# Kernel tuning notes

Hardware: AMD Instinct MI355X
Metric: run time of the kernel (lower is better)

## Reference

```python
import jax, jax.numpy as jnp
import numpy as np

EPS = 1e-5


def gcn_conv(x, src, dst, n_nodes, W, b):
    # x: [B, N, Fin]; src/dst: [E+N] (self loops included); W: [Fout, Fin]
    h = jnp.einsum('bnf,of->bno', x, W)                      # [B, N, Fout]
    deg = jnp.zeros((n_nodes,), h.dtype).at[dst].add(1.0)    # in-degree of A+I
    dinv = jnp.where(deg > 0, 1.0 / jnp.sqrt(deg), 0.0)
    norm = dinv[src] * dinv[dst]                             # [E+N]
    msg = h[:, src, :] * norm[None, :, None]                 # gather along node axis
    out = jnp.zeros_like(h).at[:, dst, :].add(msg)           # scatter-add aggregate
    return out + b


def batchnorm_nodes(x, gamma, beta):
    # torch BatchNorm1d(N) on [B, N, C]: channel axis is N, stats over (B, C)
    mean = jnp.mean(x, axis=(0, 2), keepdims=True)
    var = jnp.mean(jnp.square(x - mean), axis=(0, 2), keepdims=True)
    xn = (x - mean) * jax.lax.rsqrt(var + EPS)
    return xn * gamma[None, :, None] + beta[None, :, None]


def setup_inputs() -> dict:
    key = jax.random.key(0)
    ks = jax.random.split(key, 20)
    B, N, FIN, D, OUT, E = 4096, 64, 67, 2048, 2, 512
    s = 0.1
    d = {}
    d['x_fingerprints'] = jax.random.normal(ks[0], (B, D), jnp.float32)
    d['x_node_features'] = jax.random.normal(ks[1], (B, N, FIN), jnp.float32)
    d['edge_list'] = jax.random.randint(ks[2], (2, E), 0, N)
    d['W1'] = jax.random.normal(ks[3], (64, FIN), jnp.float32) * s
    d['b1'] = jax.random.normal(ks[4], (64,), jnp.float32) * s
    d['g1'] = 1.0 + jax.random.normal(ks[5], (N,), jnp.float32) * s
    d['be1'] = jax.random.normal(ks[6], (N,), jnp.float32) * s
    d['W2'] = jax.random.normal(ks[7], (32, 64), jnp.float32) * s
    d['b2'] = jax.random.normal(ks[8], (32,), jnp.float32) * s
    d['g2'] = 1.0 + jax.random.normal(ks[9], (N,), jnp.float32) * s
    d['be2'] = jax.random.normal(ks[10], (N,), jnp.float32) * s
    d['Wl1'] = jax.random.normal(ks[11], (400, D), jnp.float32) * (s / 4)
    d['bl1'] = jax.random.normal(ks[12], (400,), jnp.float32) * s
    d['Wl2'] = jax.random.normal(ks[13], (64, 400), jnp.float32) * s
    d['bl2'] = jax.random.normal(ks[14], (64,), jnp.float32) * s
    d['Wfc'] = jax.random.normal(ks[15], (OUT, 96), jnp.float32) * s
    d['bfc'] = jax.random.normal(ks[16], (OUT,), jnp.float32) * s
    return d


def reference(x_fingerprints, x_node_features, edge_list, W1, b1, g1, be1,
              W2, b2, g2, be2, Wl1, bl1, Wl2, bl2, Wfc, bfc):
    B, N, _ = x_node_features.shape
    loops = jnp.arange(N)
    src = jnp.concatenate([edge_list[0], loops])  # add self loops (GCNConv default)
    dst = jnp.concatenate([edge_list[1], loops])
    g = gcn_conv(x_node_features, src, dst, N, W1, b1)
    g = jax.nn.relu(batchnorm_nodes(g, g1, be1))
    g = gcn_conv(g, src, dst, N, W2, b2)
    g = jax.nn.relu(batchnorm_nodes(g, g2, be2))           # [B, N, 32]
    pooled = jnp.max(g, axis=1)                             # global_max_pool -> [B, 32]
    h = jax.nn.relu(x_fingerprints @ Wl1.T + bl1)
    h = jax.nn.relu(h @ Wl2.T + bl2)                        # [B, 64]
    out = jnp.concatenate([pooled, h], axis=1) @ Wfc.T + bfc
    return out
```

## Files before the change

### kernel.cpp

```cpp
#include <hip/hip_runtime.h>
#include <hip/hip_bf16.h>
#include <math.h>

typedef __bf16 bf16;
typedef __attribute__((ext_vector_type(8))) __bf16 bf16x8;
typedef __attribute__((ext_vector_type(4))) __bf16 bf16x4;
typedef __attribute__((ext_vector_type(4))) float f32x4;

#define EPSBN 1e-5f
#define B_    4096
#define N_    64
#define FIN_  67
#define E_    512
#define NSLOT 128

__device__ inline bf16x8 pack8(f32x4 lo, f32x4 hi) {
    bf16x8 r;
    r[0] = (bf16)lo[0]; r[1] = (bf16)lo[1]; r[2] = (bf16)lo[2]; r[3] = (bf16)lo[3];
    r[4] = (bf16)hi[0]; r[5] = (bf16)hi[1]; r[6] = (bf16)hi[2]; r[7] = (bf16)hi[3];
    return r;
}

__global__ __launch_bounds__(256) void k0_prep(const int* __restrict__ edge,
    const float* __restrict__ W1, const float* __restrict__ W2,
    float* __restrict__ partials,
    bf16* __restrict__ an_hi, bf16* __restrict__ an_lo,
    bf16* __restrict__ wpad,
    bf16* __restrict__ w2pad)
{
    int tid = threadIdx.x;
    for (int i = blockIdx.x * 256 + tid; i < NSLOT * 64 * 4; i += gridDim.x * 256)
        partials[i] = 0.f;
    if (blockIdx.x == 1) {
        for (int i = tid; i < 64 * 104; i += 256) {
            int n = i / 104, f = i % 104;
            wpad[i] = (f < FIN_) ? (bf16)W1[n * FIN_ + f] : (bf16)0.f;
        }
        return;
    }
    if (blockIdx.x == 2) {
        for (int i = tid; i < 32 * 72; i += 256) {
            int o = i / 72, f = i % 72;
            w2pad[i] = (f < 64) ? (bf16)W2[o * 64 + f] : (bf16)0.f;
        }
        return;
    }
    if (blockIdx.x != 0) return;

    __shared__ float An[64 * 64];
    __shared__ int ssrc[E_], sdst[E_];
    __shared__ int deg[N_];
    __shared__ float dinv[N_];
    for (int i = tid; i < 64 * 64; i += 256) An[i] = 0.f;
    for (int i = tid; i < E_; i += 256) { ssrc[i] = edge[i]; sdst[i] = edge[E_ + i]; }
    if (tid < N_) deg[tid] = 1;
    __syncthreads();
    for (int i = tid; i < E_; i += 256) atomicAdd(&deg[sdst[i]], 1);
    __syncthreads();
    if (tid < N_) dinv[tid] = rsqrtf((float)deg[tid]);
    __syncthreads();
    for (int i = tid; i < E_; i += 256) {
        int s = ssrc[i], d = sdst[i];
        atomicAdd(&An[d * 64 + s], dinv[s] * dinv[d]);
    }
    if (tid < N_) atomicAdd(&An[tid * 64 + tid], dinv[tid] * dinv[tid]);
    __syncthreads();
    for (int i = tid; i < 64 * 64; i += 256) {
        float v = An[i];
        bf16 h = (bf16)v;
        an_hi[i] = h;
        an_lo[i] = (bf16)(v - (float)h);
    }
}

__global__ __launch_bounds__(256, 3) void k1_gcn1(
    const float* __restrict__ x,
    const float* __restrict__ b1,
    const bf16* __restrict__ an_hi, const bf16* __restrict__ an_lo,
    const bf16* __restrict__ wpad,
    bf16* __restrict__ g1out,
    float* __restrict__ part1)
{
    __shared__ union {
        float xraw[4352];
        struct { bf16 hhi[64 * 72]; bf16 hlo[64 * 72]; } h;
    } u;
    __shared__ bf16 ost[64 * 72];

    int tid = threadIdx.x;
    int w = tid >> 6, lane = tid & 63, q = lane >> 4, r15 = lane & 15;
    int arow = w * 16 + r15;

    bf16x8 wf[3][4];
#pragma unroll
    for (int kt = 0; kt < 3; ++kt)
#pragma unroll
        for (int nt = 0; nt < 4; ++nt)
            wf[kt][nt] = *(const bf16x8*)&wpad[(nt * 16 + r15) * 104 + kt * 32 + q * 8];

    const bf16* ahp = an_hi + arow * 64 + q * 8;
    const bf16* alp = an_lo + arow * 64 + q * 8;
    bf16x8 Ah0 = *(const bf16x8*)ahp;
    bf16x8 Ah1 = *(const bf16x8*)(ahp + 32);
    bf16x8 Al0 = *(const bf16x8*)alp;
    bf16x8 Al1 = *(const bf16x8*)(alp + 32);

    float bc[4];
#pragma unroll
    for (int nt = 0; nt < 4; ++nt) bc[nt] = b1[nt * 16 + r15];

    size_t b0 = (size_t)blockIdx.x * 4;
    const f32x4* xb4 = (const f32x4*)(x + b0 * 4288);

    f32x4 pre0 = xb4[tid], pre1 = xb4[tid + 256], pre2 = xb4[tid + 512], pre3 = xb4[tid + 768];
    f32x4 pre4 = {0.f, 0.f, 0.f, 0.f};
    if (tid < 48) pre4 = xb4[tid + 1024];

    f32x4* xl4 = (f32x4*)u.xraw;
    f32x4 z4 = {0.f, 0.f, 0.f, 0.f};

#pragma unroll 1
    for (int g = 0; g < 4; ++g) {
        int b = (int)b0 + g;
        xl4[tid] = pre0; xl4[tid + 256] = pre1; xl4[tid + 512] = pre2; xl4[tid + 768] = pre3;
        if (tid < 48) xl4[tid + 1024] = pre4;
        __syncthreads();

        f32x4 acc[4] = {z4, z4, z4, z4};
        const float* xr = u.xraw + arow * FIN_;
#pragma unroll
        for (int kt = 0; kt < 3; ++kt) {
            bf16x8 a;
            if (kt < 2) {
                int k0 = kt * 32 + q * 8;
#pragma unroll
                for (int j = 0; j < 8; ++j) a[j] = (bf16)xr[k0 + j];
            } else {
#pragma unroll
                for (int j = 0; j < 8; ++j) a[j] = (bf16)0.f;
                if (q == 0) { a[0] = (bf16)xr[64]; a[1] = (bf16)xr[65]; a[2] = (bf16)xr[66]; }
            }
#pragma unroll
            for (int nt = 0; nt < 4; ++nt)
                acc[nt] = __builtin_amdgcn_mfma_f32_16x16x32_bf16(a, wf[kt][nt], acc[nt], 0, 0, 0);
        }
        if (g < 3) {
            const f32x4* xn = xb4 + (size_t)(g + 1) * 1072;
            pre0 = xn[tid]; pre1 = xn[tid + 256]; pre2 = xn[tid + 512]; pre3 = xn[tid + 768];
            if (tid < 48) pre4 = xn[tid + 1024];
        }
        __syncthreads();

        int sbase = w * 16 + q * 4;
#pragma unroll
        for (int nt = 0; nt < 4; ++nt) {
            int c = nt * 16 + r15;
            bf16x4 hi, lo;
#pragma unroll
            for (int r = 0; r < 4; ++r) {
                float v = acc[nt][r];
                bf16 h = (bf16)v;
                hi[r] = h; lo[r] = (bf16)(v - (float)h);
            }
            *(bf16x4*)&u.h.hhi[c * 72 + sbase] = hi;
            *(bf16x4*)&u.h.hlo[c * 72 + sbase] = lo;
        }
        __syncthreads();

        f32x4 acc2[4] = {z4, z4, z4, z4};
#pragma unroll
        for (int kt = 0; kt < 2; ++kt) {
            bf16x8 Ahk = kt ? Ah1 : Ah0;
            bf16x8 Alk = kt ? Al1 : Al0;
#pragma unroll
            for (int nt = 0; nt < 4; ++nt) {
                int o = (nt * 16 + r15) * 72 + kt * 32 + q * 8;
                bf16x8 Hh = *(const bf16x8*)&u.h.hhi[o];
                bf16x8 Hl = *(const bf16x8*)&u.h.hlo[o];
                acc2[nt] = __builtin_amdgcn_mfma_f32_16x16x32_bf16(Ahk, Hh, acc2[nt], 0, 0, 0);
                acc2[nt] = __builtin_amdgcn_mfma_f32_16x16x32_bf16(Ahk, Hl, acc2[nt], 0, 0, 0);
                acc2[nt] = __builtin_amdgcn_mfma_f32_16x16x32_bf16(Alk, Hh, acc2[nt], 0, 0, 0);
            }
        }
#pragma unroll
        for (int nt = 0; nt < 4; ++nt) {
            int c = nt * 16 + r15;
#pragma unroll
            for (int r = 0; r < 4; ++r)
                ost[(sbase + r) * 72 + c] = (bf16)(acc2[nt][r] + bc[nt]);
        }
        __syncthreads();

        int n = tid >> 2, oq = tid & 3;
        bf16x8 o0 = *(const bf16x8*)&ost[n * 72 + oq * 16];
        bf16x8 o1 = *(const bf16x8*)&ost[n * 72 + oq * 16 + 8];
        bf16* gp = g1out + ((size_t)b * 4096 + n * 64 + oq * 16);
        *(bf16x8*)gp = o0;
        *(bf16x8*)(gp + 8) = o1;
        float s1 = 0.f, s2 = 0.f;
#pragma unroll
        for (int j = 0; j < 8; ++j) {
            float v0 = (float)o0[j], v1 = (float)o1[j];
            s1 += v0 + v1; s2 += v0 * v0 + v1 * v1;
        }
        s1 += __shfl_xor(s1, 1); s1 += __shfl_xor(s1, 2);
        s2 += __shfl_xor(s2, 1); s2 += __shfl_xor(s2, 2);
        if (oq == 0) {
            int slot = b & (NSLOT - 1);
            atomicAdd(&part1[(slot * 64 + n) * 2 + 0], s1);
            atomicAdd(&part1[(slot * 64 + n) * 2 + 1], s2);
        }
    }
}

__global__ __launch_bounds__(64) void k_bnstats(
    const float* __restrict__ part,
    const float* __restrict__ gamma, const float* __restrict__ beta,
    float* __restrict__ scale, float* __restrict__ shift, float inv_count)
{
    int n = blockIdx.x, t = threadIdx.x;
    float s1 = part[(t * 64 + n) * 2] + part[((t + 64) * 64 + n) * 2];
    float s2 = part[(t * 64 + n) * 2 + 1] + part[((t + 64) * 64 + n) * 2 + 1];
#pragma unroll
    for (int o = 32; o > 0; o >>= 1) { s1 += __shfl_down(s1, o); s2 += __shfl_down(s2, o); }
    if (t == 0) {
        float mean = s1 * inv_count;
        float var = s2 * inv_count - mean * mean;
        float sc = gamma[n] * rsqrtf(var + EPSBN);
        scale[n] = sc;
        shift[n] = beta[n] - mean * sc;
    }
}

__global__ __launch_bounds__(256, 4) void k3_gcn2(
    const bf16* __restrict__ g1out,
    const float* __restrict__ b2,
    const float* __restrict__ scale1, const float* __restrict__ shift1,
    const bf16* __restrict__ an_hi, const bf16* __restrict__ an_lo,
    const bf16* __restrict__ w2pad,
    bf16* __restrict__ g2out,
    float* __restrict__ part2)
{
    __shared__ bf16 ya[64 * 72];
    __shared__ bf16 hhi[32 * 72];
    __shared__ bf16 hlo[32 * 72];
    __shared__ bf16 ost[64 * 40];

    int tid = threadIdx.x;
    int w = tid >> 6, lane = tid & 63, q = lane >> 4, r15 = lane & 15;
    int arow = w * 16 + r15;

    bf16x8 wf[2][2];
#pragma unroll
    for (int kt = 0; kt < 2; ++kt)
#pragma unroll
        for (int nt = 0; nt < 2; ++nt)
            wf[kt][nt] = *(const bf16x8*)&w2pad[(nt * 16 + r15) * 72 + kt * 32 + q * 8];

    const bf16* ahp = an_hi + arow * 64 + q * 8;
    const bf16* alp = an_lo + arow * 64 + q * 8;
    bf16x8 Ah0 = *(const bf16x8*)ahp;
    bf16x8 Ah1 = *(const bf16x8*)(ahp + 32);
    bf16x8 Al0 = *(const bf16x8*)alp;
    bf16x8 Al1 = *(const bf16x8*)(alp + 32);
    float sc = scale1[arow], sh = shift1[arow];
    float bc[2] = { b2[r15], b2[16 + r15] };

    size_t b0 = (size_t)blockIdx.x * 4;
    const bf16x8* gg8 = (const bf16x8*)(g1out + b0 * 4096);
    bf16x8 p0 = gg8[tid], p1 = gg8[tid + 256];

    int r0 = tid >> 3, c0 = (tid & 7) * 8;
    f32x4 z4 = {0.f, 0.f, 0.f, 0.f};

#pragma unroll 1
    for (int g = 0; g < 4; ++g) {
        int b = (int)b0 + g;
        *(bf16x8*)&ya[r0 * 72 + c0] = p0;
        *(bf16x8*)&ya[(r0 + 32) * 72 + c0] = p1;
        __syncthreads();

        f32x4 acc[2] = {z4, z4};
#pragma unroll
        for (int kt = 0; kt < 2; ++kt) {
            int k0 = kt * 32 + q * 8;
            bf16x8 raw = *(const bf16x8*)&ya[arow * 72 + k0];
            bf16x8 a;
#pragma unroll
            for (int j = 0; j < 8; ++j)
                a[j] = (bf16)fmaxf(fmaf(sc, (float)raw[j], sh), 0.f);
#pragma unroll
            for (int nt = 0; nt < 2; ++nt)
                acc[nt] = __builtin_amdgcn_mfma_f32_16x16x32_bf16(a, wf[kt][nt], acc[nt], 0, 0, 0);
        }
        if (g < 3) {
            p0 = gg8[(size_t)(g + 1) * 512 + tid];
            p1 = gg8[(size_t)(g + 1) * 512 + tid + 256];
        }
        __syncthreads();

        int sbase = w * 16 + q * 4;
#pragma unroll
        for (int nt = 0; nt < 2; ++nt) {
            int c = nt * 16 + r15;
            bf16x4 hi, lo;
#pragma unroll
            for (int r = 0; r < 4; ++r) {
                float v = acc[nt][r];
                bf16 h = (bf16)v;
                hi[r] = h; lo[r] = (bf16)(v - (float)h);
            }
            *(bf16x4*)&hhi[c * 72 + sbase] = hi;
            *(bf16x4*)&hlo[c * 72 + sbase] = lo;
        }
        __syncthreads();

        f32x4 acc2[2] = {z4, z4};
#pragma unroll
        for (int kt = 0; kt < 2; ++kt) {
            bf16x8 Ahk = kt ? Ah1 : Ah0;
            bf16x8 Alk = kt ? Al1 : Al0;
#pragma unroll
            for (int nt = 0; nt < 2; ++nt) {
                int o = (nt * 16 + r15) * 72 + kt * 32 + q * 8;
                bf16x8 Hh = *(const bf16x8*)&hhi[o];
                bf16x8 Hl = *(const bf16x8*)&hlo[o];
                acc2[nt] = __builtin_amdgcn_mfma_f32_16x16x32_bf16(Ahk, Hh, acc2[nt], 0, 0, 0);
                acc2[nt] = __builtin_amdgcn_mfma_f32_16x16x32_bf16(Ahk, Hl, acc2[nt], 0, 0, 0);
                acc2[nt] = __builtin_amdgcn_mfma_f32_16x16x32_bf16(Alk, Hh, acc2[nt], 0, 0, 0);
            }
        }
#pragma unroll
        for (int nt = 0; nt < 2; ++nt) {
            int c = nt * 16 + r15;
#pragma unroll
            for (int r = 0; r < 4; ++r)
                ost[(sbase + r) * 40 + c] = (bf16)(acc2[nt][r] + bc[nt]);
        }
        __syncthreads();

        int n = tid >> 2, oq = tid & 3;
        bf16x8 ov = *(const bf16x8*)&ost[n * 40 + oq * 8];
        *(bf16x8*)(g2out + ((size_t)b * 2048 + n * 32 + oq * 8)) = ov;
        float s1 = 0.f, s2 = 0.f;
#pragma unroll
        for (int j = 0; j < 8; ++j) {
            float v = (float)ov[j];
            s1 += v; s2 += v * v;
        }
        s1 += __shfl_xor(s1, 1); s1 += __shfl_xor(s1, 2);
        s2 += __shfl_xor(s2, 1); s2 += __shfl_xor(s2, 2);
        if (oq == 0) {
            int slot = b & (NSLOT - 1);
            atomicAdd(&part2[(slot * 64 + n) * 2 + 0], s1);
            atomicAdd(&part2[(slot * 64 + n) * 2 + 1], s2);
        }
    }
}

__global__ __launch_bounds__(256, 4) void k6_mlp1(
    const float* __restrict__ A,
    const float* __restrict__ Bw,
    float* __restrict__ part)
{
    __shared__ bf16 Bs[2][64 * 72];
    int tid = threadIdx.x;
    int m0 = blockIdx.x * 64, n0 = blockIdx.y * 64, ks = blockIdx.z;
    int w = tid >> 6, lane = tid & 63, q = lane >> 4, r15 = lane & 15;
    int brow = tid >> 2, bs8 = (tid & 3) * 16;
    bool bvalid = (n0 + brow) < 400;
    const float* pA = A + (size_t)(m0 + w * 16 + r15) * 2048 + ks * 512 + q * 8;
    const float* pB = Bw + (size_t)(n0 + brow) * 2048 + ks * 512 + bs8;
    f32x4 z4 = {0.f, 0.f, 0.f, 0.f};
    f32x4 acc[4] = {z4, z4, z4, z4};

    f32x4 a0 = *(const f32x4*)pA,        a1 = *(const f32x4*)(pA + 4);
    f32x4 a2 = *(const f32x4*)(pA + 32), a3 = *(const f32x4*)(pA + 36);
    f32x4 b0 = z4, b1 = z4, b2 = z4, b3 = z4;
    if (bvalid) {
        b0 = *(const f32x4*)pB;       b1 = *(const f32x4*)(pB + 4);
        b2 = *(const f32x4*)(pB + 8); b3 = *(const f32x4*)(pB + 12);
    }
    *(bf16x8*)&Bs[0][brow * 72 + bs8]     = pack8(b0, b1);
    *(bf16x8*)&Bs[0][brow * 72 + bs8 + 8] = pack8(b2, b3);
    __syncthreads();

#pragma unroll
    for (int t = 0; t < 8; ++t) {
        f32x4 na0, na1, na2, na3;
        f32x4 nb0 = z4, nb1 = z4, nb2 = z4, nb3 = z4;
        if (t < 7) {
            const float* qA = pA + (t + 1) * 64;
            na0 = *(const f32x4*)qA;        na1 = *(const f32x4*)(qA + 4);
            na2 = *(const f32x4*)(qA + 32); na3 = *(const f32x4*)(qA + 36);
            if (bvalid) {
                const float* qB = pB + (t + 1) * 64;
                nb0 = *(const f32x4*)qB;       nb1 = *(const f32x4*)(qB + 4);
                nb2 = *(const f32x4*)(qB + 8); nb3 = *(const f32x4*)(qB + 12);
            }
        }
        bf16x8 af0 = pack8(a0, a1), af1 = pack8(a2, a3);
        const bf16* cur = Bs[t & 1];
#pragma unroll
        for (int nt = 0; nt < 4; ++nt) {
            bf16x8 bb = *(const bf16x8*)&cur[(nt * 16 + r15) * 72 + q * 8];
            acc[nt] = __builtin_amdgcn_mfma_f32_16x16x32_bf16(af0, bb, acc[nt], 0, 0, 0);
        }
#pragma unroll
        for (int nt = 0; nt < 4; ++nt) {
            bf16x8 bb = *(const bf16x8*)&cur[(nt * 16 + r15) * 72 + 32 + q * 8];
            acc[nt] = __builtin_amdgcn_mfma_f32_16x16x32_bf16(af1, bb, acc[nt], 0, 0, 0);
        }
        if (t < 7) {
            bf16* nxt = (bf16*)Bs[(t & 1) ^ 1];
            *(bf16x8*)&nxt[brow * 72 + bs8]     = pack8(nb0, nb1);
            *(bf16x8*)&nxt[brow * 72 + bs8 + 8] = pack8(nb2, nb3);
            __syncthreads();
            a0 = na0; a1 = na1; a2 = na2; a3 = na3;
        }
    }
    float* pp = part + (size_t)ks * 1638400;
#pragma unroll
    for (int nt = 0; nt < 4; ++nt)
#pragma unroll
        for (int r = 0; r < 4; ++r) {
            int mm = m0 + w * 16 + q * 4 + r;
            int nn = n0 + nt * 16 + r15;
            if (nn < 400) pp[(size_t)mm * 400 + nn] = acc[nt][r];
        }
}

__global__ __launch_bounds__(256) void k7_mlp2(
    const float* __restrict__ part,
    const float* __restrict__ bl1,
    const float* __restrict__ Bw,
    const float* __restrict__ bias,
    float* __restrict__ Cout)
{
    __shared__ bf16 As[16 * 416];
    int tid = threadIdx.x;
    int m0 = blockIdx.x * 16;
    for (int i = tid; i < 800; i += 256) {
        int rr = i / 50, cc = (i % 50) * 8;
        const float* p0 = part + (size_t)(m0 + rr) * 400 + cc;
        f32x4 x0 = *(const f32x4*)p0,             x1 = *(const f32x4*)(p0 + 4);
        f32x4 y0 = *(const f32x4*)(p0 + 1638400), y1 = *(const f32x4*)(p0 + 1638404);
        f32x4 u0 = *(const f32x4*)(p0 + 3276800), u1 = *(const f32x4*)(p0 + 3276804);
        f32x4 v0 = *(const f32x4*)(p0 + 4915200), v1 = *(const f32x4*)(p0 + 4915204);
        f32x4 w0 = *(const f32x4*)&bl1[cc],       w1 = *(const f32x4*)&bl1[cc + 4];
        bf16x8 o;
#pragma unroll
        for (int j = 0; j < 4; ++j) {
            o[j]     = (bf16)fmaxf(x0[j] + y0[j] + u0[j] + v0[j] + w0[j], 0.f);
            o[4 + j] = (bf16)fmaxf(x1[j] + y1[j] + u1[j] + v1[j] + w1[j], 0.f);
        }
        *(bf16x8*)&As[rr * 416 + cc] = o;
    }
    if (tid < 32) {
        int rr = tid >> 1, cc = 400 + (tid & 1) * 8;
        bf16x8 z;
#pragma unroll
        for (int k = 0; k < 8; ++k) z[k] = (bf16)0.f;
        *(bf16x8*)&As[rr * 416 + cc] = z;
    }
    __syncthreads();

    int w = tid >> 6, lane = tid & 63, q = lane >> 4, r15 = lane & 15;
    f32x4 acc = {0.f, 0.f, 0.f, 0.f};
    const float* pB = Bw + (size_t)(w * 16 + r15) * 400;
#pragma unroll 4
    for (int kt = 0; kt < 13; ++kt) {
        int k0 = kt * 32 + q * 8;
        bf16x8 a = *(const bf16x8*)&As[r15 * 416 + k0];
        bf16x8 bb;
#pragma unroll
        for (int k = 0; k < 8; ++k) bb[k] = (bf16)0.f;
        if (k0 < 400) {
            f32x4 c0 = *(const f32x4*)(pB + k0);
            f32x4 c1 = *(const f32x4*)(pB + k0 + 4);
            bb[0] = (bf16)c0[0]; bb[1] = (bf16)c0[1]; bb[2] = (bf16)c0[2]; bb[3] = (bf16)c0[3];
            bb[4] = (bf16)c1[0]; bb[5] = (bf16)c1[1]; bb[6] = (bf16)c1[2]; bb[7] = (bf16)c1[3];
        }
        acc = __builtin_amdgcn_mfma_f32_16x16x32_bf16(a, bb, acc, 0, 0, 0);
    }
#pragma unroll
    for (int r = 0; r < 4; ++r) {
        int mm = m0 + q * 4 + r;
        int nn = w * 16 + r15;
        float v = fmaxf(acc[r] + bias[nn], 0.f);
        Cout[(size_t)mm * 64 + nn] = v;
    }
}

__global__ __launch_bounds__(256) void k8_final(
    const bf16* __restrict__ g2out,
    const float* __restrict__ scale2, const float* __restrict__ shift2,
    const float* __restrict__ h2,
    const float* __restrict__ Wfc,
    const float* __restrict__ bfc,
    float* __restrict__ out)
{
    __shared__ float s2s[64], sh2s[64];
    int tid = threadIdx.x;
    if (tid < 64) { s2s[tid] = scale2[tid]; sh2s[tid] = shift2[tid]; }
    __syncthreads();
    int w = tid >> 6, lane = tid & 63;
    int b = blockIdx.x * 4 + w;
    int c = lane & 31, half = lane >> 5;
    const bf16* gb = g2out + (size_t)b * 2048;
    float mx = 0.f;
    for (int i = 0; i < 32; ++i) {
        int n = half * 32 + i;
        float v = (float)gb[n * 32 + c];
        float val = fmaf(s2s[n], v, sh2s[n]);
        mx = fmaxf(mx, val);
    }
    mx = fmaxf(mx, __shfl_xor(mx, 32));
    float h2v = h2[(size_t)b * 64 + lane];
#pragma unroll
    for (int o = 0; o < 2; ++o) {
        float t = h2v * Wfc[o * 96 + 32 + lane];
        if (half == 0) t += mx * Wfc[o * 96 + c];
#pragma unroll
        for (int off = 32; off > 0; off >>= 1) t += __shfl_xor(t, off);
        if (lane == 0) out[(size_t)b * 2 + o] = t + bfc[o];
    }
}

extern "C" void kernel_launch(void* const* d_in, const int* in_sizes, int n_in,
                              void* d_out, int out_size, void* d_ws, size_t ws_size,
                              hipStream_t stream)
{
    const float* x_fp   = (const float*)d_in[0];
    const float* x_node = (const float*)d_in[1];
    const int*   edge   = (const int*)d_in[2];
    const float* W1     = (const float*)d_in[3];
    const float* b1     = (const float*)d_in[4];
    const float* g1     = (const float*)d_in[5];
    const float* be1    = (const float*)d_in[6];
    const float* W2     = (const float*)d_in[7];
    const float* b2     = (const float*)d_in[8];
    const float* g2     = (const float*)d_in[9];
    const float* be2    = (const float*)d_in[10];
    const float* Wl1    = (const float*)d_in[11];
    const float* bl1    = (const float*)d_in[12];
    const float* Wl2    = (const float*)d_in[13];
    const float* bl2    = (const float*)d_in[14];
    const float* Wfc    = (const float*)d_in[15];
    const float* bfc    = (const float*)d_in[16];
    float* out = (float*)d_out;

    char* ws = (char*)d_ws;
    float* scale1  = (float*)(ws + 5632);
    float* shift1  = (float*)(ws + 5888);
    float* scale2  = (float*)(ws + 6144);
    float* shift2  = (float*)(ws + 6400);
    float* part1   = (float*)(ws + 8192);
    float* part2   = (float*)(ws + 8192 + 65536);
    bf16*  g1out   = (bf16*)(ws + 139264);
    float* part6   = (float*)(ws + 139264);
    bf16*  g2out   = (bf16*)(ws + 33693696ull);
    float* h2      = (float*)(ws + 53747712ull);
    bf16*  an_hi   = (bf16*)(ws + 53747712ull);
    bf16*  an_lo   = (bf16*)(ws + 53747712ull + 8192);
    bf16*  wpad    = (bf16*)(ws + 53747712ull + 16384);
    bf16*  w2pad   = (bf16*)(ws + 53747712ull + 32768);

    k0_prep<<<dim3(64), dim3(256), 0, stream>>>(edge, W1, W2, part1, an_hi, an_lo, wpad, w2pad);
    k1_gcn1<<<dim3(1024), dim3(256), 0, stream>>>(x_node, b1, an_hi, an_lo, wpad, g1out, part1);
    k_bnstats<<<dim3(64), dim3(64), 0, stream>>>(part1, g1, be1, scale1, shift1,
                                                 1.f / (4096.f * 64.f));
    k3_gcn2<<<dim3(1024), dim3(256), 0, stream>>>(g1out, b2, scale1, shift1,
                                                  an_hi, an_lo, w2pad, g2out, part2);
    k_bnstats<<<dim3(64), dim3(64), 0, stream>>>(part2, g2, be2, scale2, shift2,
                                                 1.f / (4096.f * 32.f));
    k6_mlp1<<<dim3(64, 7, 4), dim3(256), 0, stream>>>(x_fp, Wl1, part6);
    k7_mlp2<<<dim3(256), dim3(256), 0, stream>>>(part6, bl1, Wl2, bl2, h2);
    k8_final<<<dim3(1024), dim3(256), 0, stream>>>(g2out, scale2, shift2, h2, Wfc, bfc, out);
}
```

Measured before the change: 247.3 us.

## Stage full K-slice of Wl1 in LDS and double M tile in mlp1

The first fingerprint MLP GEMM kernel now loads the block's entire 64x512 bf16 weight slice into shared memory once, removing the per-step double-buffered weight loads and barriers. Each block now covers 128 rows instead of 64, so every weight fragment read from LDS feeds two MFMAs, and the grid is halved. Activation loads are prefetched two steps ahead in registers. In exchange the kernel uses about 65KB of LDS and more registers, and the launch bound drops to 2 blocks per CU, which lowers occupancy.

```diff
diff --git a/kernel.cpp b/kernel.cpp
--- a/kernel.cpp
+++ b/kernel.cpp
@@ -358,76 +358,85 @@
     }
 }
 
-__global__ __launch_bounds__(256, 4) void k6_mlp1(
+__global__ __launch_bounds__(256, 2) void k6_mlp1(
     const float* __restrict__ A,
     const float* __restrict__ Bw,
     float* __restrict__ part)
 {
-    __shared__ bf16 Bs[2][64 * 72];
+    __shared__ bf16 Bs[64 * 520];
     int tid = threadIdx.x;
-    int m0 = blockIdx.x * 64, n0 = blockIdx.y * 64, ks = blockIdx.z;
+    int m0 = blockIdx.x * 128, n0 = blockIdx.y * 64, ks = blockIdx.z;
+    f32x4 z4 = {0.f, 0.f, 0.f, 0.f};
+
+#pragma unroll
+    for (int i = 0; i < 16; ++i) {
+        int idx = i * 256 + tid;
+        int row = idx >> 6, col = (idx & 63) * 8;
+        f32x4 lo = z4, hi = z4;
+        if (n0 + row < 400) {
+            const float* p = Bw + (size_t)(n0 + row) * 2048 + ks * 512 + col;
+            lo = *(const f32x4*)p; hi = *(const f32x4*)(p + 4);
+        }
+        *(bf16x8*)&Bs[row * 520 + col] = pack8(lo, hi);
+    }
+    __syncthreads();
+
     int w = tid >> 6, lane = tid & 63, q = lane >> 4, r15 = lane & 15;
-    int brow = tid >> 2, bs8 = (tid & 3) * 16;
-    bool bvalid = (n0 + brow) < 400;
-    const float* pA = A + (size_t)(m0 + w * 16 + r15) * 2048 + ks * 512 + q * 8;
-    const float* pB = Bw + (size_t)(n0 + brow) * 2048 + ks * 512 + bs8;
-    f32x4 z4 = {0.f, 0.f, 0.f, 0.f};
-    f32x4 acc[4] = {z4, z4, z4, z4};
-
-    f32x4 a0 = *(const f32x4*)pA,        a1 = *(const f32x4*)(pA + 4);
-    f32x4 a2 = *(const f32x4*)(pA + 32), a3 = *(const f32x4*)(pA + 36);
-    f32x4 b0 = z4, b1 = z4, b2 = z4, b3 = z4;
-    if (bvalid) {
-        b0 = *(const f32x4*)pB;       b1 = *(const f32x4*)(pB + 4);
-        b2 = *(const f32x4*)(pB + 8); b3 = *(const f32x4*)(pB + 12);
-    }
-    *(bf16x8*)&Bs[0][brow * 72 + bs8]     = pack8(b0, b1);
-    *(bf16x8*)&Bs[0][brow * 72 + bs8 + 8] = pack8(b2, b3);
-    __syncthreads();
+    const float* pA0 = A + (size_t)(m0 + w * 16 + r15) * 2048 + ks * 512 + q * 8;
+    const float* pA1 = pA0 + 64 * 2048;
+
+    f32x4 acc0[4] = {z4, z4, z4, z4};
+    f32x4 acc1[4] = {z4, z4, z4, z4};
+    f32x4 abuf[2][8];
+
+#define LOADA(slot, t)                                                        \
+    do {                                                                      \
+        const float* _p0 = pA0 + (t) * 64;                                    \
+        const float* _p1 = pA1 + (t) * 64;                                    \
+        abuf[slot][0] = *(const f32x4*)_p0;       abuf[slot][1] = *(const f32x4*)(_p0 + 4);  \
+        abuf[slot][2] = *(const f32x4*)(_p0 + 32); abuf[slot][3] = *(const f32x4*)(_p0 + 36); \
+        abuf[slot][4] = *(const f32x4*)_p1;       abuf[slot][5] = *(const f32x4*)(_p1 + 4);  \
+        abuf[slot][6] = *(const f32x4*)(_p1 + 32); abuf[slot][7] = *(const f32x4*)(_p1 + 36); \
+    } while (0)
+
+    LOADA(0, 0);
+    LOADA(1, 1);
 
 #pragma unroll
     for (int t = 0; t < 8; ++t) {
-        f32x4 na0, na1, na2, na3;
-        f32x4 nb0 = z4, nb1 = z4, nb2 = z4, nb3 = z4;
-        if (t < 7) {
-            const float* qA = pA + (t + 1) * 64;
-            na0 = *(const f32x4*)qA;        na1 = *(const f32x4*)(qA + 4);
-            na2 = *(const f32x4*)(qA + 32); na3 = *(const f32x4*)(qA + 36);
-            if (bvalid) {
-                const float* qB = pB + (t + 1) * 64;
-                nb0 = *(const f32x4*)qB;       nb1 = *(const f32x4*)(qB + 4);
-                nb2 = *(const f32x4*)(qB + 8); nb3 = *(const f32x4*)(qB + 12);
+        const int sl = t & 1;
+        bf16x8 af00 = pack8(abuf[sl][0], abuf[sl][1]);
+        bf16x8 af10 = pack8(abuf[sl][2], abuf[sl][3]);
+        bf16x8 af01 = pack8(abuf[sl][4], abuf[sl][5]);
+        bf16x8 af11 = pack8(abuf[sl][6], abuf[sl][7]);
+        if (t < 6) LOADA(sl, t + 2);
+        const bf16* bt = Bs + t * 64;
+#pragma unroll
+        for (int nt = 0; nt < 4; ++nt) {
+            const bf16* br = bt + (nt * 16 + r15) * 520 + q * 8;
+            bf16x8 bb0 = *(const bf16x8*)br;
+            acc0[nt] = __builtin_amdgcn_mfma_f32_16x16x32_bf16(af00, bb0, acc0[nt], 0, 0, 0);
+            acc1[nt] = __builtin_amdgcn_mfma_f32_16x16x32_bf16(af01, bb0, acc1[nt], 0, 0, 0);
+            bf16x8 bb1 = *(const bf16x8*)(br + 32);
+            acc0[nt] = __builtin_amdgcn_mfma_f32_16x16x32_bf16(af10, bb1, acc0[nt], 0, 0, 0);
+            acc1[nt] = __builtin_amdgcn_mfma_f32_16x16x32_bf16(af11, bb1, acc1[nt], 0, 0, 0);
+        }
+    }
+#undef LOADA
+
+    float* pp = part + (size_t)ks * 1638400;
+#pragma unroll
+    for (int nt = 0; nt < 4; ++nt) {
+        int nn = n0 + nt * 16 + r15;
+        if (nn < 400) {
+#pragma unroll
+            for (int r = 0; r < 4; ++r) {
+                int mm = m0 + w * 16 + q * 4 + r;
+                pp[(size_t)mm * 400 + nn] = acc0[nt][r];
+                pp[(size_t)(mm + 64) * 400 + nn] = acc1[nt][r];
             }
         }
-        bf16x8 af0 = pack8(a0, a1), af1 = pack8(a2, a3);
-        const bf16* cur = Bs[t & 1];
-#pragma unroll
-        for (int nt = 0; nt < 4; ++nt) {
-            bf16x8 bb = *(const bf16x8*)&cur[(nt * 16 + r15) * 72 + q * 8];
-            acc[nt] = __builtin_amdgcn_mfma_f32_16x16x32_bf16(af0, bb, acc[nt], 0, 0, 0);
-        }
-#pragma unroll
-        for (int nt = 0; nt < 4; ++nt) {
-            bf16x8 bb = *(const bf16x8*)&cur[(nt * 16 + r15) * 72 + 32 + q * 8];
-            acc[nt] = __builtin_amdgcn_mfma_f32_16x16x32_bf16(af1, bb, acc[nt], 0, 0, 0);
-        }
-        if (t < 7) {
-            bf16* nxt = (bf16*)Bs[(t & 1) ^ 1];
-            *(bf16x8*)&nxt[brow * 72 + bs8]     = pack8(nb0, nb1);
-            *(bf16x8*)&nxt[brow * 72 + bs8 + 8] = pack8(nb2, nb3);
-            __syncthreads();
-            a0 = na0; a1 = na1; a2 = na2; a3 = na3;
-        }
-    }
-    float* pp = part + (size_t)ks * 1638400;
-#pragma unroll
-    for (int nt = 0; nt < 4; ++nt)
-#pragma unroll
-        for (int r = 0; r < 4; ++r) {
-            int mm = m0 + w * 16 + q * 4 + r;
-            int nn = n0 + nt * 16 + r15;
-            if (nn < 400) pp[(size_t)mm * 400 + nn] = acc[nt][r];
-        }
+    }
 }
 
 __global__ __launch_bounds__(256) void k7_mlp2(
@@ -574,7 +583,7 @@
                                                   an_hi, an_lo, w2pad, g2out, part2);
     k_bnstats<<<dim3(64), dim3(64), 0, stream>>>(part2, g2, be2, scale2, shift2,
                                                  1.f / (4096.f * 32.f));
-    k6_mlp1<<<dim3(64, 7, 4), dim3(256), 0, stream>>>(x_fp, Wl1, part6);
+    k6_mlp1<<<dim3(32, 7, 4), dim3(256), 0, stream>>>(x_fp, Wl1, part6);
     k7_mlp2<<<dim3(256), dim3(256), 0, stream>>>(part6, bl1, Wl2, bl2, h2);
     k8_final<<<dim3(1024), dim3(256), 0, stream>>>(g2out, scale2, shift2, h2, Wfc, bfc, out);
 }
```

After: 255.7 us. 1.03x slower.

## Stage both MLP1 operands through LDS with a two-deep register prefetch

Applied to the files above, without the earlier changes.

Restructures the first fingerprint-MLP GEMM kernel so that A and B tiles are both loaded coalesced, one row per four threads, and staged through single-buffered LDS in K-steps of 32. Loads run two steps ahead in registers, and two barriers per step replace the earlier double-buffered B-only scheme where A was read straight from global memory. The occupancy hint of 4 blocks is also dropped from launch bounds. The goal is better global coalescing for A, at the price of more barriers and smaller K-steps per sync.

```diff
diff --git a/kernel.cpp b/kernel.cpp
--- a/kernel.cpp
+++ b/kernel.cpp
@@ -358,67 +358,58 @@
     }
 }
 
-__global__ __launch_bounds__(256, 4) void k6_mlp1(
+__global__ __launch_bounds__(256) void k6_mlp1(
     const float* __restrict__ A,
     const float* __restrict__ Bw,
     float* __restrict__ part)
 {
-    __shared__ bf16 Bs[2][64 * 72];
+    __shared__ bf16 As[64 * 36];
+    __shared__ bf16 Bs[64 * 36];
     int tid = threadIdx.x;
     int m0 = blockIdx.x * 64, n0 = blockIdx.y * 64, ks = blockIdx.z;
+    int row = tid >> 2, seg = tid & 3;
     int w = tid >> 6, lane = tid & 63, q = lane >> 4, r15 = lane & 15;
-    int brow = tid >> 2, bs8 = (tid & 3) * 16;
-    bool bvalid = (n0 + brow) < 400;
-    const float* pA = A + (size_t)(m0 + w * 16 + r15) * 2048 + ks * 512 + q * 8;
-    const float* pB = Bw + (size_t)(n0 + brow) * 2048 + ks * 512 + bs8;
     f32x4 z4 = {0.f, 0.f, 0.f, 0.f};
     f32x4 acc[4] = {z4, z4, z4, z4};
-
-    f32x4 a0 = *(const f32x4*)pA,        a1 = *(const f32x4*)(pA + 4);
-    f32x4 a2 = *(const f32x4*)(pA + 32), a3 = *(const f32x4*)(pA + 36);
-    f32x4 b0 = z4, b1 = z4, b2 = z4, b3 = z4;
-    if (bvalid) {
-        b0 = *(const f32x4*)pB;       b1 = *(const f32x4*)(pB + 4);
-        b2 = *(const f32x4*)(pB + 8); b3 = *(const f32x4*)(pB + 12);
-    }
-    *(bf16x8*)&Bs[0][brow * 72 + bs8]     = pack8(b0, b1);
-    *(bf16x8*)&Bs[0][brow * 72 + bs8 + 8] = pack8(b2, b3);
-    __syncthreads();
-
-#pragma unroll
-    for (int t = 0; t < 8; ++t) {
-        f32x4 na0, na1, na2, na3;
-        f32x4 nb0 = z4, nb1 = z4, nb2 = z4, nb3 = z4;
-        if (t < 7) {
-            const float* qA = pA + (t + 1) * 64;
-            na0 = *(const f32x4*)qA;        na1 = *(const f32x4*)(qA + 4);
-            na2 = *(const f32x4*)(qA + 32); na3 = *(const f32x4*)(qA + 36);
-            if (bvalid) {
-                const float* qB = pB + (t + 1) * 64;
-                nb0 = *(const f32x4*)qB;       nb1 = *(const f32x4*)(qB + 4);
-                nb2 = *(const f32x4*)(qB + 8); nb3 = *(const f32x4*)(qB + 12);
-            }
-        }
-        bf16x8 af0 = pack8(a0, a1), af1 = pack8(a2, a3);
-        const bf16* cur = Bs[t & 1];
+    const float* pA = A + (size_t)(m0 + row) * 2048 + ks * 512 + seg * 8;
+    bool bvalid = (n0 + row) < 400;
+    const float* pB = Bw + (size_t)(n0 + row) * 2048 + ks * 512 + seg * 8;
+
+    f32x4 a[2][2], c[2][2];
+    c[0][0] = z4; c[0][1] = z4; c[1][0] = z4; c[1][1] = z4;
+
+#define LD(s, t)                                                              \
+    do {                                                                      \
+        const float* _a = pA + (t) * 32;                                      \
+        a[s][0] = *(const f32x4*)_a; a[s][1] = *(const f32x4*)(_a + 4);       \
+        if (bvalid) {                                                         \
+            const float* _b = pB + (t) * 32;                                  \
+            c[s][0] = *(const f32x4*)_b; c[s][1] = *(const f32x4*)(_b + 4);   \
+        }                                                                     \
+    } while (0)
+
+    LD(0, 0);
+    LD(1, 1);
+
+#pragma unroll
+    for (int kt = 0; kt < 16; ++kt) {
+        const int sl = kt & 1;
+        bf16x8 apk = pack8(a[sl][0], a[sl][1]);
+        bf16x8 bpk = pack8(c[sl][0], c[sl][1]);
+        __syncthreads();
+        *(bf16x8*)&As[row * 36 + seg * 8] = apk;
+        *(bf16x8*)&Bs[row * 36 + seg * 8] = bpk;
+        __syncthreads();
+        if (kt < 14) LD(sl, kt + 2);
+        bf16x8 af = *(const bf16x8*)&As[(w * 16 + r15) * 36 + q * 8];
 #pragma unroll
         for (int nt = 0; nt < 4; ++nt) {
-            bf16x8 bb = *(const bf16x8*)&cur[(nt * 16 + r15) * 72 + q * 8];
-            acc[nt] = __builtin_amdgcn_mfma_f32_16x16x32_bf16(af0, bb, acc[nt], 0, 0, 0);
-        }
-#pragma unroll
-        for (int nt = 0; nt < 4; ++nt) {
-            bf16x8 bb = *(const bf16x8*)&cur[(nt * 16 + r15) * 72 + 32 + q * 8];
-            acc[nt] = __builtin_amdgcn_mfma_f32_16x16x32_bf16(af1, bb, acc[nt], 0, 0, 0);
-        }
-        if (t < 7) {
-            bf16* nxt = (bf16*)Bs[(t & 1) ^ 1];
-            *(bf16x8*)&nxt[brow * 72 + bs8]     = pack8(nb0, nb1);
-            *(bf16x8*)&nxt[brow * 72 + bs8 + 8] = pack8(nb2, nb3);
-            __syncthreads();
-            a0 = na0; a1 = na1; a2 = na2; a3 = na3;
-        }
-    }
+            bf16x8 bb = *(const bf16x8*)&Bs[(nt * 16 + r15) * 36 + q * 8];
+            acc[nt] = __builtin_amdgcn_mfma_f32_16x16x32_bf16(af, bb, acc[nt], 0, 0, 0);
+        }
+    }
+#undef LD
+
     float* pp = part + (size_t)ks * 1638400;
 #pragma unroll
     for (int nt = 0; nt < 4; ++nt)
```

New measurement: 246.1 us. No clear change (-0.5%).
